# Optimization experiments

Hardware: AMD Instinct MI355X
Metric: run time of the kernel (lower is better)

The kernel has to match this reference:

```python
import jax, jax.numpy as jnp
import numpy as np

B, I, O = 128, 256, 4096
DECAY = 0.95


def setup_inputs() -> dict:
    key = jax.random.key(0)
    k_x, k_stim, k_a = jax.random.split(key, 3)
    return {
        "x": jax.random.normal(k_x, (B, I), dtype=jnp.float32),
        "stim": jax.random.normal(k_stim, (O, I), dtype=jnp.float32),
        "a": jax.random.normal(k_a, (O,), dtype=jnp.float32),
        "b": jnp.ones((O,), dtype=jnp.float32),
        "state": jnp.zeros((B, O), dtype=jnp.float32),
    }


def reference(x, stim, a, b, state):
    # L-inf distance between every input row and every stimulus row.
    # (B, 1, I) - (1, O, I) -> (B, O, I); max over input dim -> (B, O)
    distances = jnp.max(jnp.abs(x[:, None, :] - stim[None, :, :]), axis=-1)
    value = jax.nn.sigmoid((a[None, :] - distances) * b[None, :])  # (B, O)
    new_state = state * DECAY + value
    return new_state
```

## Files before the change

### kernel.cpp

```cpp
#include <hip/hip_runtime.h>
#include <math.h>

#define BB 128
#define II 256
#define OO 4096
#define DECAY 0.95f

constexpr int TB  = 16;
constexpr int TO  = 64;
constexpr int PAD = 4;
constexpr int LDW = II + PAD;

__global__ __launch_bounds__(256) void stimulus_linf_kernel(
    const float* __restrict__ x,
    const float* __restrict__ stim,
    const float* __restrict__ a,
    const float* __restrict__ b,
    const float* __restrict__ state,
    float* __restrict__ out)
{
    __shared__ float s_stim[TO][LDW];

    const int tid  = threadIdx.x;
    const int lane = tid & 63;
    const int wave = tid >> 6;

    const int o_tile  = blockIdx.x & 63;
    const int bi_tile = blockIdx.x >> 6;
    const int o_base  = o_tile * TO;
    const int bi_base = bi_tile * TB;

    const int wrow = __builtin_amdgcn_readfirstlane(bi_base + wave * 4);

    const int o   = o_base + lane;
    const float av = a[o];
    const float bv = b[o];
    float st[4];
    #pragma unroll
    for (int r = 0; r < 4; ++r)
        st[r] = state[(bi_base + wave * 4 + r) * OO + o];

    const float4* xr0 = reinterpret_cast<const float4*>(x + (wrow + 0) * II);
    const float4* xr1 = reinterpret_cast<const float4*>(x + (wrow + 1) * II);
    const float4* xr2 = reinterpret_cast<const float4*>(x + (wrow + 2) * II);
    const float4* xr3 = reinterpret_cast<const float4*>(x + (wrow + 3) * II);

    float d[4] = {0.f, 0.f, 0.f, 0.f};

    auto stage = [&](int h) {
        #pragma unroll
        for (int k = 0; k < 8; ++k) {
            const int idx = tid + k * 256;
            const int row = idx >> 5;
            const int col = h * 128 + (idx & 31) * 4;
            const float4 v = *reinterpret_cast<const float4*>(
                &stim[(o_base + row) * II + col]);
            *reinterpret_cast<float4*>(&s_stim[row][col]) = v;
        }
    };

    auto compute = [&](int i4lo, int i4hi) {
        #pragma unroll 8
        for (int i4 = i4lo; i4 < i4hi; ++i4) {
            const float4 s4 =
                *reinterpret_cast<const float4*>(&s_stim[lane][i4 * 4]);
            const float4 xv0 = xr0[i4];
            const float4 xv1 = xr1[i4];
            const float4 xv2 = xr2[i4];
            const float4 xv3 = xr3[i4];
            d[0] = fmaxf(fmaxf(d[0], fabsf(xv0.x - s4.x)), fabsf(xv0.y - s4.y));
            d[0] = fmaxf(fmaxf(d[0], fabsf(xv0.z - s4.z)), fabsf(xv0.w - s4.w));
            d[1] = fmaxf(fmaxf(d[1], fabsf(xv1.x - s4.x)), fabsf(xv1.y - s4.y));
            d[1] = fmaxf(fmaxf(d[1], fabsf(xv1.z - s4.z)), fabsf(xv1.w - s4.w));
            d[2] = fmaxf(fmaxf(d[2], fabsf(xv2.x - s4.x)), fabsf(xv2.y - s4.y));
            d[2] = fmaxf(fmaxf(d[2], fabsf(xv2.z - s4.z)), fabsf(xv2.w - s4.w));
            d[3] = fmaxf(fmaxf(d[3], fabsf(xv3.x - s4.x)), fabsf(xv3.y - s4.y));
            d[3] = fmaxf(fmaxf(d[3], fabsf(xv3.z - s4.z)), fabsf(xv3.w - s4.w));
        }
    };

    stage(0);
    __syncthreads();
    stage(1);
    compute(0, 32);
    __syncthreads();
    compute(32, 64);

    #pragma unroll
    for (int r = 0; r < 4; ++r) {
        const int bi = bi_base + wave * 4 + r;
        const float z   = (av - d[r]) * bv;
        const float val = 1.f / (1.f + __expf(-z));
        out[bi * OO + o] = st[r] * DECAY + val;
    }
}

extern "C" void kernel_launch(void* const* d_in, const int* in_sizes, int n_in,
                              void* d_out, int out_size, void* d_ws, size_t ws_size,
                              hipStream_t stream) {
    const float* x     = (const float*)d_in[0];
    const float* stim  = (const float*)d_in[1];
    const float* a     = (const float*)d_in[2];
    const float* b     = (const float*)d_in[3];
    const float* state = (const float*)d_in[4];
    float* out = (float*)d_out;

    const dim3 grid((OO / TO) * (BB / TB));
    const dim3 block(256);
    stimulus_linf_kernel<<<grid, block, 0, stream>>>(x, stim, a, b, state, out);
}
```

Before: 73.42 us.

## Stage x in LDS, halve output tile, and double-buffer stimulus in four chunks

Each block now loads its 16 rows of x into shared memory instead of having each wave read x from global memory. The stimulus tile is cut to 32 outputs and streamed in four 64-column chunks through a double buffer. The two halves of each wave split the input dimension and combine their maxima with a cross-lane shuffle. This doubles the grid size and lowers LDS use per block, aiming for higher occupancy and less global traffic, at the cost of extra barriers, duplicated LDS reads of x, and a shuffle reduction.

Result: no change. 73.09 us (-0.4%).

```diff
diff --git a/kernel.cpp b/kernel.cpp
--- a/kernel.cpp
+++ b/kernel.cpp
@@ -6,12 +6,12 @@
 #define OO 4096
 #define DECAY 0.95f
 
-constexpr int TB  = 16;
-constexpr int TO  = 64;
-constexpr int PAD = 4;
-constexpr int LDW = II + PAD;
+constexpr int TB = 16;
+constexpr int TO = 32;
+constexpr int QC = 64;
+constexpr int SP = QC + 4;
 
-__global__ __launch_bounds__(256) void stimulus_linf_kernel(
+__global__ __launch_bounds__(256, 4) void stimulus_linf_kernel(
     const float* __restrict__ x,
     const float* __restrict__ stim,
     const float* __restrict__ a,
@@ -19,55 +19,65 @@
     const float* __restrict__ state,
     float* __restrict__ out)
 {
-    __shared__ float s_stim[TO][LDW];
+    __shared__ float s_stim[2][TO][SP];
+    __shared__ float s_x[TB][II];
 
     const int tid  = threadIdx.x;
     const int lane = tid & 63;
     const int wave = tid >> 6;
+    const int ol   = lane & 31;
+    const int h2   = lane >> 5;
 
-    const int o_tile  = blockIdx.x & 63;
-    const int bi_tile = blockIdx.x >> 6;
+    const int o_tile  = blockIdx.x & 127;
+    const int bi_tile = blockIdx.x >> 7;
     const int o_base  = o_tile * TO;
     const int bi_base = bi_tile * TB;
 
-    const int wrow = __builtin_amdgcn_readfirstlane(bi_base + wave * 4);
-
-    const int o   = o_base + lane;
+    const int o  = o_base + ol;
     const float av = a[o];
     const float bv = b[o];
-    float st[4];
+    const int r0 = h2 * 2;
+    const float st0 = state[(bi_base + wave * 4 + r0    ) * OO + o];
+    const float st1 = state[(bi_base + wave * 4 + r0 + 1) * OO + o];
+
     #pragma unroll
-    for (int r = 0; r < 4; ++r)
-        st[r] = state[(bi_base + wave * 4 + r) * OO + o];
+    for (int k = 0; k < 4; ++k) {
+        const int idx = tid + k * 256;
+        const int row = idx >> 6;
+        const int c4  = (idx & 63) * 4;
+        *reinterpret_cast<float4*>(&s_x[row][c4]) =
+            *reinterpret_cast<const float4*>(&x[(bi_base + row) * II + c4]);
+    }
 
-    const float4* xr0 = reinterpret_cast<const float4*>(x + (wrow + 0) * II);
-    const float4* xr1 = reinterpret_cast<const float4*>(x + (wrow + 1) * II);
-    const float4* xr2 = reinterpret_cast<const float4*>(x + (wrow + 2) * II);
-    const float4* xr3 = reinterpret_cast<const float4*>(x + (wrow + 3) * II);
+    auto stage = [&](int q, int bq) {
+        #pragma unroll
+        for (int k = 0; k < 2; ++k) {
+            const int idx = tid + k * 256;
+            const int row = idx >> 4;
+            const int c4  = (idx & 15) * 4;
+            *reinterpret_cast<float4*>(&s_stim[bq][row][c4]) =
+                *reinterpret_cast<const float4*>(
+                    &stim[(o_base + row) * II + q * QC + c4]);
+        }
+    };
 
     float d[4] = {0.f, 0.f, 0.f, 0.f};
 
-    auto stage = [&](int h) {
-        #pragma unroll
-        for (int k = 0; k < 8; ++k) {
-            const int idx = tid + k * 256;
-            const int row = idx >> 5;
-            const int col = h * 128 + (idx & 31) * 4;
-            const float4 v = *reinterpret_cast<const float4*>(
-                &stim[(o_base + row) * II + col]);
-            *reinterpret_cast<float4*>(&s_stim[row][col]) = v;
-        }
-    };
-
-    auto compute = [&](int i4lo, int i4hi) {
-        #pragma unroll 8
-        for (int i4 = i4lo; i4 < i4hi; ++i4) {
-            const float4 s4 =
-                *reinterpret_cast<const float4*>(&s_stim[lane][i4 * 4]);
-            const float4 xv0 = xr0[i4];
-            const float4 xv1 = xr1[i4];
-            const float4 xv2 = xr2[i4];
-            const float4 xv3 = xr3[i4];
+    auto compute = [&](int q, int bq) {
+        const int cbase = h2 * 32;
+        const int xbase = q * QC + cbase;
+        #pragma unroll 4
+        for (int i4 = 0; i4 < 8; ++i4) {
+            const float4 s4 = *reinterpret_cast<const float4*>(
+                &s_stim[bq][ol][cbase + i4 * 4]);
+            const float4 xv0 = *reinterpret_cast<const float4*>(
+                &s_x[wave * 4 + 0][xbase + i4 * 4]);
+            const float4 xv1 = *reinterpret_cast<const float4*>(
+                &s_x[wave * 4 + 1][xbase + i4 * 4]);
+            const float4 xv2 = *reinterpret_cast<const float4*>(
+                &s_x[wave * 4 + 2][xbase + i4 * 4]);
+            const float4 xv3 = *reinterpret_cast<const float4*>(
+                &s_x[wave * 4 + 3][xbase + i4 * 4]);
             d[0] = fmaxf(fmaxf(d[0], fabsf(xv0.x - s4.x)), fabsf(xv0.y - s4.y));
             d[0] = fmaxf(fmaxf(d[0], fabsf(xv0.z - s4.z)), fabsf(xv0.w - s4.w));
             d[1] = fmaxf(fmaxf(d[1], fabsf(xv1.x - s4.x)), fabsf(xv1.y - s4.y));
@@ -79,19 +89,31 @@
         }
     };
 
-    stage(0);
+    stage(0, 0);
     __syncthreads();
-    stage(1);
-    compute(0, 32);
+    stage(1, 1);
+    compute(0, 0);
     __syncthreads();
-    compute(32, 64);
+    stage(2, 0);
+    compute(1, 1);
+    __syncthreads();
+    stage(3, 1);
+    compute(2, 0);
+    __syncthreads();
+    compute(3, 1);
 
     #pragma unroll
-    for (int r = 0; r < 4; ++r) {
-        const int bi = bi_base + wave * 4 + r;
+    for (int r = 0; r < 4; ++r)
+        d[r] = fmaxf(d[r], __shfl_xor(d[r], 32, 64));
+
+    #pragma unroll
+    for (int rr = 0; rr < 2; ++rr) {
+        const int r   = r0 + rr;
+        const int bi  = bi_base + wave * 4 + r;
         const float z   = (av - d[r]) * bv;
         const float val = 1.f / (1.f + __expf(-z));
-        out[bi * OO + o] = st[r] * DECAY + val;
+        const float s   = (rr == 0) ? st0 : st1;
+        out[bi * OO + o] = s * DECAY + val;
     }
 }
 
```
